# Kernel tuning notes

Measured on AMD Instinct MI355X. Metric: run time of the kernel, lower is better.

## Reference

```python
import jax, jax.numpy as jnp
import numpy as np

B, S, I, H = 64, 1024, 1024, 1024


def setup_inputs() -> dict:
    key = jax.random.key(0)
    ks = jax.random.split(key, 14)
    bound = (1.0 / H) ** 0.5
    u = lambda k, shape: jax.random.uniform(k, shape, jnp.float32, -bound, bound)
    return {
        "inputs": jax.random.normal(ks[0], (B, S, I), jnp.float32),
        "hidden_states": jax.random.normal(ks[1], (1, B, H), jnp.float32),
        "w_ir": u(ks[2], (H, I)), "w_iz": u(ks[3], (H, I)), "w_in": u(ks[4], (H, I)),
        "b_ir": u(ks[5], (H,)), "b_iz": u(ks[6], (H,)), "b_in": u(ks[7], (H,)),
        "w_hr": u(ks[8], (H, H)), "w_hz": u(ks[9], (H, H)), "w_hn": u(ks[10], (H, H)),
        "b_hr": u(ks[11], (H,)), "b_hz": u(ks[12], (H,)), "b_hn": u(ks[13], (H,)),
    }


def reference(inputs, hidden_states, w_ir, w_iz, w_in, b_ir, b_iz, b_in,
              w_hr, w_hz, w_hn, b_hr, b_hz, b_hn):
    # Precompute input projections for all timesteps (batched GEMMs), [B,S,H]
    x_ir = jnp.einsum('bsi,hi->bsh', inputs, w_ir) + b_ir
    x_iz = jnp.einsum('bsi,hi->bsh', inputs, w_iz) + b_iz
    x_in = jnp.einsum('bsi,hi->bsh', inputs, w_in) + b_in

    def step(h, xs):
        xr, xz, xn = xs  # each [B,H]
        r = jax.nn.sigmoid(xr + h @ w_hr.T + b_hr)
        z = jax.nn.sigmoid(xz + h @ w_hz.T + b_hz)
        n = jnp.tanh(xn + r * (h @ w_hn.T + b_hn))
        h_new = (1.0 - z) * n + z * h
        return h_new, h_new

    h0 = hidden_states[0]  # [B,H]
    # scan over time: xs leading axis S
    xs = (jnp.swapaxes(x_ir, 0, 1), jnp.swapaxes(x_iz, 0, 1), jnp.swapaxes(x_in, 0, 1))
    h_final, outs = jax.lax.scan(step, h0, xs)
    outputs = jnp.swapaxes(outs, 0, 1)  # [B,S,H]
    return outputs, h_final[None]
```

## Files before the change

kernel.cpp:

```cpp
#include <hip/hip_runtime.h>
#include <hip/hip_bf16.h>

typedef __attribute__((ext_vector_type(8))) short bf16x8;
typedef __attribute__((ext_vector_type(4))) float f32x4;
typedef unsigned short u16;
typedef unsigned int u32;

static constexpr int B_ = 64, S_ = 1024, I_ = 1024, H_ = 1024;

__device__ __forceinline__ u16 f2b(float f) {
  union { float f; unsigned u; } v; v.f = f;
  unsigned r = v.u + 0x7FFF + ((v.u >> 16) & 1);
  return (u16)(r >> 16);
}
__device__ __forceinline__ float b2f(u16 u) {
  union { unsigned u; float f; } v; v.u = ((unsigned)u) << 16;
  return v.f;
}

__device__ __forceinline__ void st_coh_u16(void* p, unsigned v) {
  asm volatile("global_store_short %0, %1, off sc0 sc1" :: "v"(p), "v"(v) : "memory");
}
__device__ __forceinline__ void st_coh_u32(void* p, unsigned v) {
  asm volatile("global_store_dword %0, %1, off sc0 sc1" :: "v"(p), "v"(v) : "memory");
}
__device__ __forceinline__ unsigned ld_coh_u32_wait(const void* p) {
  unsigned r;
  asm volatile("global_load_dword %0, %1, off sc0 sc1\n\ts_waitcnt vmcnt(0)"
               : "=v"(r) : "v"(p) : "memory");
  return r;
}
__device__ __forceinline__ uint4 ld_coh_b128(const void* p) {
  uint4 r;
  asm volatile("global_load_dwordx4 %0, %1, off sc0 sc1" : "=v"(r) : "v"(p) : "memory");
  return r;
}

__global__ void cvt_f32_bf16(const float* __restrict__ src, u16* __restrict__ dst, int n4) {
  int i = blockIdx.x * blockDim.x + threadIdx.x;
  int stride = gridDim.x * blockDim.x;
  for (; i < n4; i += stride) {
    float4 f = ((const float4*)src)[i];
    ushort4 o;
    o.x = f2b(f.x); o.y = f2b(f.y); o.z = f2b(f.z); o.w = f2b(f.w);
    ((ushort4*)dst)[i] = o;
  }
}

__global__ __launch_bounds__(256) void xproj_gemm(
    const u16* __restrict__ A, const u16* __restrict__ W,
    const float* __restrict__ b_ir, const float* __restrict__ b_iz, const float* __restrict__ b_in,
    u16* __restrict__ X) {
  __shared__ u16 smem[16384];
  u16* As = smem;
  u16* Bs = smem + 8192;
  int bid = blockIdx.x;
  int mt = bid / 24; int rr = bid % 24; int g = rr >> 3; int nt = rr & 7;
  int tid = threadIdx.x, lane = tid & 63, wid = tid >> 6;
  int wr = wid >> 1, wc = wid & 1;
  const u16* A0 = A + (size_t)mt * 128 * 1024;
  const u16* W0 = W + (size_t)g * 1024 * 1024 + (size_t)nt * 128 * 1024;
  f32x4 acc[4][4] = {};
  for (int k0 = 0; k0 < 1024; k0 += 64) {
    __syncthreads();
#pragma unroll
    for (int j = 0; j < 4; ++j) {
      int c = wid * 4 + j;
      int row = c * 8 + (lane >> 3);
      int ke = (lane & 7) * 8;
      __builtin_amdgcn_global_load_lds(
          (const __attribute__((address_space(1))) void*)(A0 + row * 1024 + k0 + ke),
          (__attribute__((address_space(3))) void*)(As + c * 512), 16, 0, 0);
      __builtin_amdgcn_global_load_lds(
          (const __attribute__((address_space(1))) void*)(W0 + row * 1024 + k0 + ke),
          (__attribute__((address_space(3))) void*)(Bs + c * 512), 16, 0, 0);
    }
    asm volatile("s_waitcnt vmcnt(0)" ::: "memory");
    __syncthreads();
#pragma unroll
    for (int kk = 0; kk < 64; kk += 32) {
      bf16x8 a[4], b[4];
      int rbase = lane & 15;
      int koff = kk + ((lane >> 4) << 3);
#pragma unroll
      for (int mi = 0; mi < 4; ++mi)
        a[mi] = *(const bf16x8*)(As + (wr * 64 + mi * 16 + rbase) * 64 + koff);
#pragma unroll
      for (int ni = 0; ni < 4; ++ni)
        b[ni] = *(const bf16x8*)(Bs + (wc * 64 + ni * 16 + rbase) * 64 + koff);
#pragma unroll
      for (int mi = 0; mi < 4; ++mi)
#pragma unroll
        for (int ni = 0; ni < 4; ++ni)
          acc[mi][ni] = __builtin_amdgcn_mfma_f32_16x16x32_bf16(a[mi], b[ni], acc[mi][ni], 0, 0, 0);
    }
  }
  __syncthreads();
  const float* bp = (g == 0) ? b_ir : (g == 1) ? b_iz : b_in;
  float bias[4];
#pragma unroll
  for (int ni = 0; ni < 4; ++ni)
    bias[ni] = bp[nt * 128 + wc * 64 + ni * 16 + (lane & 15)];
#pragma unroll
  for (int mi = 0; mi < 4; ++mi)
#pragma unroll
    for (int ni = 0; ni < 4; ++ni) {
      int ml = wr * 64 + mi * 16 + ((lane >> 4) << 2);
      int nl = wc * 64 + ni * 16 + (lane & 15);
#pragma unroll
      for (int i = 0; i < 4; ++i)
        smem[(ml + i) * 128 + nl] = f2b(acc[mi][ni][i] + bias[ni]);
    }
  __syncthreads();
#pragma unroll
  for (int j = 0; j < 8; ++j) {
    int c = tid + j * 256;
    int rowl = c >> 4;
    int n0 = (c & 15) * 8;
    int m = mt * 128 + rowl;
    int b = m >> 10, s = m & 1023;
    bf16x8 v = *(const bf16x8*)(smem + rowl * 128 + n0);
    *(bf16x8*)(X + ((size_t)((s * 64 + b) * 3 + g)) * 1024 + nt * 128 + n0) = v;
  }
}

__global__ __launch_bounds__(256) void gru_scan(
    const u16* __restrict__ xbuf, const float* __restrict__ h0p,
    const float* __restrict__ w_hr, const float* __restrict__ w_hz, const float* __restrict__ w_hn,
    const float* __restrict__ b_hr, const float* __restrict__ b_hz, const float* __restrict__ b_hn,
    u16* __restrict__ hbf, float* __restrict__ out, u32* __restrict__ flags) {
  extern __shared__ u16 smem[];
  u16* Wl = smem;
  u16* Hl = smem + 49152;
  float* ex = (float*)Hl;
  int tid = threadIdx.x, lane = tid & 63, wid = tid >> 6;
  int wg = blockIdx.x, mq = wg & 3, cb = wg >> 2;
  u32* gflags = flags + mq * 64;

  for (int idx = tid; idx < 3 * 2048; idx += 256) {
    int g = idx >> 11; int rem = idx & 2047; int row = rem >> 7; int ch = rem & 127;
    const float* wsrc = (g == 0) ? w_hr : (g == 1) ? w_hz : w_hn;
    const float* src = wsrc + (size_t)(cb * 16 + row) * 1024 + ch * 8;
    float4 f0 = *(const float4*)src;
    float4 f1 = *(const float4*)(src + 4);
    bf16x8 v;
    v[0] = (short)f2b(f0.x); v[1] = (short)f2b(f0.y); v[2] = (short)f2b(f0.z); v[3] = (short)f2b(f0.w);
    v[4] = (short)f2b(f1.x); v[5] = (short)f2b(f1.y); v[6] = (short)f2b(f1.z); v[7] = (short)f2b(f1.w);
    int kbyte = (ch * 16) ^ ((row & 7) << 4);
    *(bf16x8*)((char*)(Wl + g * 16384) + row * 2048 + kbyte) = v;
  }

  int b_l = tid >> 4, c_l = tid & 15;
  int bg = mq * 16 + b_l, cg = cb * 16 + c_l;
  float h = h0p[bg * 1024 + cg];
  float bhr = b_hr[cg], bhz = b_hz[cg], bhn = b_hn[cg];
  st_coh_u16(hbf + bg * 1024 + cg, f2b(h));
  __syncthreads();
  if (tid == 0) st_coh_u32(gflags + cb, 1u);

  const size_t outb = (size_t)bg * S_ * H_;
  for (int t = 0; t < S_; ++t) {
    const u16* rdbuf = hbf + (size_t)(t & 1) * 65536;
    u16* wrbuf = hbf + (size_t)((t + 1) & 1) * 65536;

    const u16* xp = xbuf + (size_t)(t * 64 + bg) * 3072 + cg;
    u16 xr_u = xp[0], xz_u = xp[1024], xn_u = xp[2048];

    {
      unsigned tgt = (unsigned)(t + 1);
      const u32* fp = gflags + lane;
      unsigned v = ld_coh_u32_wait(fp);
      while (!__all((int)(v >= tgt))) {
        __builtin_amdgcn_s_sleep(1);
        v = ld_coh_u32_wait(fp);
      }
    }

    uint4 tmp[8];
#pragma unroll
    for (int j = 0; j < 8; ++j) {
      int ch2 = tid + j * 256;
      int row = ch2 >> 7, kc = ch2 & 127;
      tmp[j] = ld_coh_b128(rdbuf + (mq * 16 + row) * 1024 + kc * 8);
    }
    asm volatile("s_waitcnt vmcnt(0)" ::: "memory");
    __builtin_amdgcn_sched_barrier(0);
#pragma unroll
    for (int j = 0; j < 8; ++j) {
      int ch2 = tid + j * 256;
      int row = ch2 >> 7, kc = ch2 & 127;
      int kbyte = (kc * 16) ^ ((row & 7) << 4);
      *(uint4*)((char*)Hl + row * 2048 + kbyte) = tmp[j];
    }
    __syncthreads();

    f32x4 acc0 = {}, acc1 = {}, acc2 = {}, acc3 = {};
    if (wid < 3) {
      const char* wbase = (const char*)(Wl + wid * 16384);
      const char* hbase = (const char*)Hl;
      int row = lane & 15;
      int klane = (lane >> 4) << 4;
      int sw = (row & 7) << 4;
#pragma unroll
      for (int ks = 0; ks < 32; ks += 4) {
#pragma unroll
        for (int q = 0; q < 4; ++q) {
          int off = row * 2048 + ((((ks + q) << 6) + klane) ^ sw);
          bf16x8 av = *(const bf16x8*)(hbase + off);
          bf16x8 bv = *(const bf16x8*)(wbase + off);
          if (q == 0) acc0 = __builtin_amdgcn_mfma_f32_16x16x32_bf16(av, bv, acc0, 0, 0, 0);
          else if (q == 1) acc1 = __builtin_amdgcn_mfma_f32_16x16x32_bf16(av, bv, acc1, 0, 0, 0);
          else if (q == 2) acc2 = __builtin_amdgcn_mfma_f32_16x16x32_bf16(av, bv, acc2, 0, 0, 0);
          else acc3 = __builtin_amdgcn_mfma_f32_16x16x32_bf16(av, bv, acc3, 0, 0, 0);
        }
      }
    }
    __syncthreads();
    if (wid < 3) {
      f32x4 acc = (acc0 + acc1) + (acc2 + acc3);
      int col = lane & 15, r0 = (lane >> 4) << 2;
#pragma unroll
      for (int i = 0; i < 4; ++i)
        ex[wid * 256 + (r0 + i) * 16 + col] = acc[i];
    }
    __syncthreads();

    float hr = ex[b_l * 16 + c_l] + bhr;
    float hz = ex[256 + b_l * 16 + c_l] + bhz;
    float hn = ex[512 + b_l * 16 + c_l] + bhn;
    float xr = b2f(xr_u), xz = b2f(xz_u), xn = b2f(xn_u);
    float r = 1.f / (1.f + __expf(-(xr + hr)));
    float z = 1.f / (1.f + __expf(-(xz + hz)));
    float nn = 1.f - 2.f / (__expf(2.f * (xn + r * hn)) + 1.f);
    h = (1.f - z) * nn + z * h;
    st_coh_u16(wrbuf + bg * 1024 + cg, f2b(h));
    __syncthreads();
    if (tid == 0) st_coh_u32(gflags + cb, (unsigned)(t + 2));
    out[outb + (size_t)t * H_ + cg] = h;
  }
  out[(size_t)B_ * S_ * H_ + bg * 1024 + cg] = h;
}

extern "C" void kernel_launch(void* const* d_in, const int* in_sizes, int n_in,
                              void* d_out, int out_size, void* d_ws, size_t ws_size,
                              hipStream_t stream) {
  const float* inputs = (const float*)d_in[0];
  const float* h0p    = (const float*)d_in[1];
  const float* w_ir   = (const float*)d_in[2];
  const float* w_iz   = (const float*)d_in[3];
  const float* w_in   = (const float*)d_in[4];
  const float* b_ir   = (const float*)d_in[5];
  const float* b_iz   = (const float*)d_in[6];
  const float* b_in   = (const float*)d_in[7];
  const float* w_hr   = (const float*)d_in[8];
  const float* w_hz   = (const float*)d_in[9];
  const float* w_hn   = (const float*)d_in[10];
  const float* b_hr   = (const float*)d_in[11];
  const float* b_hz   = (const float*)d_in[12];
  const float* b_hn   = (const float*)d_in[13];
  float* out = (float*)d_out;

  size_t xbytes  = (size_t)S_ * B_ * 3 * H_ * 2;
  size_t wibytes = (size_t)3 * H_ * I_ * 2;
  size_t hbytes  = (size_t)2 * B_ * H_ * 2;
  size_t flagbytes = 1024;
  if (ws_size < xbytes + wibytes + hbytes + flagbytes) return;

  u16* xbuf = (u16*)d_ws;
  u16* wibf = (u16*)((char*)d_ws + xbytes);
  u16* hbf  = (u16*)((char*)d_ws + xbytes + wibytes);
  u32* flags = (u32*)((char*)d_ws + xbytes + wibytes + hbytes);
  u16* Abf  = (u16*)d_out;

  (void)hipMemsetAsync(flags, 0, flagbytes, stream);

  cvt_f32_bf16<<<2048, 256, 0, stream>>>(inputs, Abf, B_ * S_ * I_ / 4);
  cvt_f32_bf16<<<256, 256, 0, stream>>>(w_ir, wibf,               H_ * I_ / 4);
  cvt_f32_bf16<<<256, 256, 0, stream>>>(w_iz, wibf + H_ * I_,     H_ * I_ / 4);
  cvt_f32_bf16<<<256, 256, 0, stream>>>(w_in, wibf + 2 * H_ * I_, H_ * I_ / 4);

  xproj_gemm<<<12288, 256, 0, stream>>>(Abf, wibf, b_ir, b_iz, b_in, xbuf);

  (void)hipFuncSetAttribute((const void*)gru_scan, hipFuncAttributeMaxDynamicSharedMemorySize, 131072);
  void* args[] = {(void*)&xbuf, (void*)&h0p, (void*)&w_hr, (void*)&w_hz, (void*)&w_hn,
                  (void*)&b_hr, (void*)&b_hz, (void*)&b_hn, (void*)&hbf, (void*)&out,
                  (void*)&flags};
  (void)hipLaunchCooperativeKernel((void*)gru_scan, dim3(256), dim3(256), args, 131072, stream);
}
```

Measured before the change: 4.879 ms.

## Use per-wave flags and tiled hidden-state layout to cut per-step barriers

Each wave now publishes its own completion flag after a vmcnt wait, in place of a block-wide barrier followed by one flag per workgroup. Each wave loads only the hidden rows it needs from a tiled h buffer, so waves can proceed on finer-grained dependencies. The exchange buffer gets its own LDS region, which removes one __syncthreads between the MFMA and the scatter. The cost is four times as many flags to poll and a larger LDS footprint. The launch requests 134144 bytes of shared memory while the attribute is set to 135168, which looks consistent.

```diff
diff --git a/kernel.cpp b/kernel.cpp
--- a/kernel.cpp
+++ b/kernel.cpp
@@ -132,10 +132,10 @@
   extern __shared__ u16 smem[];
   u16* Wl = smem;
   u16* Hl = smem + 49152;
-  float* ex = (float*)Hl;
+  float* ex = (float*)(smem + 65536);
   int tid = threadIdx.x, lane = tid & 63, wid = tid >> 6;
   int wg = blockIdx.x, mq = wg & 3, cb = wg >> 2;
-  u32* gflags = flags + mq * 64;
+  u32* gflags = flags + mq * 256;
 
   for (int idx = tid; idx < 3 * 2048; idx += 256) {
     int g = idx >> 11; int rem = idx & 2047; int row = rem >> 7; int ch = rem & 127;
@@ -154,21 +154,21 @@
   int bg = mq * 16 + b_l, cg = cb * 16 + c_l;
   float h = h0p[bg * 1024 + cg];
   float bhr = b_hr[cg], bhz = b_hz[cg], bhn = b_hn[cg];
-  st_coh_u16(hbf + bg * 1024 + cg, f2b(h));
-  __syncthreads();
-  if (tid == 0) st_coh_u32(gflags + cb, 1u);
+  st_coh_u16(hbf + (mq * 64 + cb) * 256 + b_l * 16 + c_l, f2b(h));
+  asm volatile("s_waitcnt vmcnt(0)" ::: "memory");
+  if (lane == 0) st_coh_u32(gflags + cb * 4 + wid, 1u);
 
   const size_t outb = (size_t)bg * S_ * H_;
   for (int t = 0; t < S_; ++t) {
-    const u16* rdbuf = hbf + (size_t)(t & 1) * 65536;
-    u16* wrbuf = hbf + (size_t)((t + 1) & 1) * 65536;
+    const u16* rbase = hbf + ((size_t)(t & 1) * 256 + mq * 64) * 256;
+    u16* wtile = hbf + (((size_t)((t + 1) & 1)) * 256 + mq * 64 + cb) * 256;
 
     const u16* xp = xbuf + (size_t)(t * 64 + bg) * 3072 + cg;
     u16 xr_u = xp[0], xz_u = xp[1024], xn_u = xp[2048];
 
     {
       unsigned tgt = (unsigned)(t + 1);
-      const u32* fp = gflags + lane;
+      const u32* fp = gflags + lane * 4 + wid;
       unsigned v = ld_coh_u32_wait(fp);
       while (!__all((int)(v >= tgt))) {
         __builtin_amdgcn_s_sleep(1);
@@ -179,17 +179,18 @@
     uint4 tmp[8];
 #pragma unroll
     for (int j = 0; j < 8; ++j) {
-      int ch2 = tid + j * 256;
-      int row = ch2 >> 7, kc = ch2 & 127;
-      tmp[j] = ld_coh_b128(rdbuf + (mq * 16 + row) * 1024 + kc * 8);
+      int l2 = lane + j * 64;
+      int p = l2 >> 3, rr = (l2 >> 1) & 3, q = l2 & 1;
+      tmp[j] = ld_coh_b128(rbase + p * 256 + (wid * 4 + rr) * 16 + q * 8);
     }
     asm volatile("s_waitcnt vmcnt(0)" ::: "memory");
     __builtin_amdgcn_sched_barrier(0);
 #pragma unroll
     for (int j = 0; j < 8; ++j) {
-      int ch2 = tid + j * 256;
-      int row = ch2 >> 7, kc = ch2 & 127;
-      int kbyte = (kc * 16) ^ ((row & 7) << 4);
+      int l2 = lane + j * 64;
+      int p = l2 >> 3, rr = (l2 >> 1) & 3, q = l2 & 1;
+      int row = wid * 4 + rr;
+      int kbyte = (p * 32 + q * 16) ^ ((row & 7) << 4);
       *(uint4*)((char*)Hl + row * 2048 + kbyte) = tmp[j];
     }
     __syncthreads();
@@ -214,9 +215,6 @@
           else acc3 = __builtin_amdgcn_mfma_f32_16x16x32_bf16(av, bv, acc3, 0, 0, 0);
         }
       }
-    }
-    __syncthreads();
-    if (wid < 3) {
       f32x4 acc = (acc0 + acc1) + (acc2 + acc3);
       int col = lane & 15, r0 = (lane >> 4) << 2;
 #pragma unroll
@@ -233,9 +231,9 @@
     float z = 1.f / (1.f + __expf(-(xz + hz)));
     float nn = 1.f - 2.f / (__expf(2.f * (xn + r * hn)) + 1.f);
     h = (1.f - z) * nn + z * h;
-    st_coh_u16(wrbuf + bg * 1024 + cg, f2b(h));
-    __syncthreads();
-    if (tid == 0) st_coh_u32(gflags + cb, (unsigned)(t + 2));
+    st_coh_u16(wtile + b_l * 16 + c_l, f2b(h));
+    asm volatile("s_waitcnt vmcnt(0)" ::: "memory");
+    if (lane == 0) st_coh_u32(gflags + cb * 4 + wid, (unsigned)(t + 2));
     out[outb + (size_t)t * H_ + cg] = h;
   }
   out[(size_t)B_ * S_ * H_ + bg * 1024 + cg] = h;
@@ -263,7 +261,7 @@
   size_t xbytes  = (size_t)S_ * B_ * 3 * H_ * 2;
   size_t wibytes = (size_t)3 * H_ * I_ * 2;
   size_t hbytes  = (size_t)2 * B_ * H_ * 2;
-  size_t flagbytes = 1024;
+  size_t flagbytes = 4096;
   if (ws_size < xbytes + wibytes + hbytes + flagbytes) return;
 
   u16* xbuf = (u16*)d_ws;
@@ -281,9 +279,9 @@
 
   xproj_gemm<<<12288, 256, 0, stream>>>(Abf, wibf, b_ir, b_iz, b_in, xbuf);
 
-  (void)hipFuncSetAttribute((const void*)gru_scan, hipFuncAttributeMaxDynamicSharedMemorySize, 131072);
+  (void)hipFuncSetAttribute((const void*)gru_scan, hipFuncAttributeMaxDynamicSharedMemorySize, 135168);
   void* args[] = {(void*)&xbuf, (void*)&h0p, (void*)&w_hr, (void*)&w_hz, (void*)&w_hn,
                   (void*)&b_hr, (void*)&b_hz, (void*)&b_hn, (void*)&hbf, (void*)&out,
                   (void*)&flags};
-  (void)hipLaunchCooperativeKernel((void*)gru_scan, dim3(256), dim3(256), args, 131072, stream);
-}
+  (void)hipLaunchCooperativeKernel((void*)gru_scan, dim3(256), dim3(256), args, 134144, stream);
+}
```

Result: slower. 5.687 ms (+16.6%).
